# Kernel tuning notes

Measured on AMD Instinct MI355X. Metric: run time of the kernel, lower is better.

Reference implementation:

```python
import jax, jax.numpy as jnp
import numpy as np
import math

B = 64; H = 768; MAXL = 256; QL = 16  # query_lengths+1
LA = MAXL + QL  # 272 token-axis padded length for branch a
NC = 3


def _sa(x, qkv_w, qkv_b, scale):
    # x: [B, L, D]; qkv_w: [3, D, D] (query, key, value); returns [B, L, D]
    q = x @ qkv_w[0] + qkv_b[0]
    k = x @ qkv_w[1] + qkv_b[1]
    v = x @ qkv_w[2] + qkv_b[2]
    attn = jax.nn.softmax(jnp.einsum('bld,bmd->blm', q, k) * scale, axis=-1)
    return jnp.einsum('blm,bmd->bld', attn, v)


def setup_inputs() -> dict:
    key = jax.random.key(0)
    ks = jax.random.split(key, 16)
    rn = lambda k, s: jax.random.normal(k, s, jnp.float32) * 0.02
    return {
        'tokens': jax.random.normal(ks[0], (B, LA + 1, H), jnp.float32),
        'cls_tokens': jax.random.normal(ks[1], (B, MAXL + 1, H), jnp.float32),
        'a_qkv_w': rn(ks[2], (3, H, H)), 'a_qkv_b': jnp.zeros((3, H), jnp.float32),
        'af_qkv_w': rn(ks[3], (3, LA, LA)), 'af_qkv_b': jnp.zeros((3, LA), jnp.float32),
        'b_qkv_w': rn(ks[4], (3, H, H)), 'b_qkv_b': jnp.zeros((3, H), jnp.float32),
        'bf_qkv_w': rn(ks[5], (3, MAXL, MAXL)), 'bf_qkv_b': jnp.zeros((3, MAXL), jnp.float32),
        'atW_w': rn(ks[6], (H, 100)), 'atW_b': jnp.zeros((100,), jnp.float32),
        'afW_w': rn(ks[7], (H, 100)), 'afW_b': jnp.zeros((100,), jnp.float32),
        'btW_w': rn(ks[8], (H, 100)), 'btW_b': jnp.zeros((100,), jnp.float32),
        'bfW_w': rn(ks[9], (H, 100)), 'bfW_b': jnp.zeros((100,), jnp.float32),
        'aft_w': rn(ks[10], (10000, 1000)), 'aft_b': jnp.zeros((1000,), jnp.float32),
        'bft_w': rn(ks[11], (10000, 1000)), 'bft_b': jnp.zeros((1000,), jnp.float32),
        'fnn1_w': rn(ks[12], (2 * H, H)), 'fnn1_b': jnp.zeros((H,), jnp.float32),
        'fnn2_w': rn(ks[13], (H, NC)), 'fnn2_b': jnp.zeros((NC,), jnp.float32),
    }


def _forward(tokens, cls_tokens, a_qkv_w, a_qkv_b, af_qkv_w, af_qkv_b,
             b_qkv_w, b_qkv_b, bf_qkv_w, bf_qkv_b,
             atW_w, atW_b, afW_w, afW_b, btW_w, btW_b, bfW_w, bfW_b,
             aft_w, aft_b, bft_w, bft_b, fnn1_w, fnn1_b, fnn2_w, fnn2_b):
    CLS = tokens[:, 0, :]
    cls_CLS = cls_tokens[:, 0, :]
    xa = tokens[:, 1:, :]
    xa = jnp.pad(xa, ((0, 0), (0, LA - xa.shape[1]), (0, 0)))  # [B, LA, H]
    xb = cls_tokens[:, 1:, :]
    xb = jnp.pad(xb, ((0, 0), (0, MAXL - xb.shape[1]), (0, 0)))  # [B, MAXL, H]

    # branch a: token-axis self-attention (TSA) + feature-axis (FSA)
    aTSA = _sa(xa, a_qkv_w, a_qkv_b, 1.0 / math.sqrt(H))                        # [B, LA, H]
    aFSA = _sa(jnp.swapaxes(xa, 1, 2), af_qkv_w, af_qkv_b, 1.0 / math.sqrt(LA))  # [B, H, LA]
    aFSA = jnp.swapaxes(aFSA, 1, 2)                                              # [B, LA, H]
    aT = aTSA @ atW_w + atW_b   # [B, LA, 100]
    aF = aFSA @ afW_w + afW_b   # [B, LA, 100]
    a_TFSA = jnp.einsum('blm,bln->bmn', aT, aF).reshape(tokens.shape[0], 10000) @ aft_w + aft_b

    # branch b
    bTSA = _sa(xb, b_qkv_w, b_qkv_b, 1.0 / math.sqrt(H))
    bFSA = _sa(jnp.swapaxes(xb, 1, 2), bf_qkv_w, bf_qkv_b, 1.0 / math.sqrt(MAXL))
    bFSA = jnp.swapaxes(bFSA, 1, 2)
    bT = bTSA @ btW_w + btW_b
    bF = bFSA @ bfW_w + bfW_b
    b_TFSA = jnp.einsum('blm,bln->bmn', bT, bF).reshape(tokens.shape[0], 10000) @ bft_w + bft_b

    # classifier head (dropout is identity in eval mode)
    h = jnp.concatenate([CLS, cls_CLS], axis=1)
    predicts = (h @ fnn1_w + fnn1_b) @ fnn2_w + fnn2_b
    # concatenate the TFSA branches so the attention math stays live (original
    # computes them but returns only predicts; see notes)
    return jnp.concatenate([predicts, a_TFSA, b_TFSA], axis=1)


def reference(tokens, cls_tokens, a_qkv_w, a_qkv_b, af_qkv_w, af_qkv_b,
              b_qkv_w, b_qkv_b, bf_qkv_w, bf_qkv_b,
              atW_w, atW_b, afW_w, afW_b, btW_w, btW_b, bfW_w, bfW_b,
              aft_w, aft_b, bft_w, bft_b, fnn1_w, fnn1_b, fnn2_w, fnn2_b):
    return _forward(tokens, cls_tokens, a_qkv_w, a_qkv_b, af_qkv_w, af_qkv_b,
                    b_qkv_w, b_qkv_b, bf_qkv_w, bf_qkv_b,
                    atW_w, atW_b, afW_w, afW_b, btW_w, btW_b, bfW_w, bfW_b,
                    aft_w, aft_b, bft_w, bft_b, fnn1_w, fnn1_b, fnn2_w, fnn2_b)
```

## Files before the change

### kernel.cpp

```cpp
#include <hip/hip_runtime.h>
#include <hip/hip_bf16.h>
#include <math.h>

typedef __hip_bfloat16 bf16;
typedef __attribute__((ext_vector_type(8))) short bf16x8;
typedef __attribute__((ext_vector_type(4))) float f32x4;

typedef const void __attribute__((address_space(1)))* gptr_t;
typedef void __attribute__((address_space(3)))* lptr_t;

static __device__ __forceinline__ void gload16(const void* g, void* l) {
    __builtin_amdgcn_global_load_lds((gptr_t)g, (lptr_t)l, 16, 0, 0);
}

static __device__ __forceinline__ float tofl(float x) { return x; }
static __device__ __forceinline__ float tofl(bf16 x) { return __bfloat162float(x); }
static __device__ __forceinline__ float bfbits(unsigned short u) {
    return __uint_as_float(((unsigned)u) << 16);
}

template<int BN>
__global__ __launch_bounds__(256)
void gemm_mfma2(const bf16* __restrict__ A, const bf16* __restrict__ B,
                const float* __restrict__ bias, void* __restrict__ C, int c_mode,
                int M, int N, int K,
                long a_batch, long lda, int a_mod,
                long b_batch, long ldb, int b_div,
                long bias_stride, long c_batch, long c_row,
                float scale, int k_chunk,
                bf16* __restrict__ Ct, long t_zbatch, long t_batch, long t_ld,
                int t_colbase, int t_rowdiv)
{
    constexpr int BM = 128;
    constexpr int WN = BN / 2;
    constexpr int FM = 4, FN = WN / 16;
    constexpr int CP = BN + 4;
    constexpr int BUFS = (BM + BN) * 32;
    constexpr int NBUF = 3;
    constexpr int P = 2 + BN / 64;
    constexpr int ABSZ = NBUF * BUFS * 2;
    constexpr int CSZ  = BM * CP * 2;
    constexpr int SMSZ = (CSZ > ABSZ) ? CSZ : ABSZ;
    __shared__ __align__(16) char smem[SMSZ];
    short* SA = (short*)smem;

    const int gx = gridDim.x, gy = gridDim.y;
    const int nwg = gx * gy * (int)gridDim.z;
    const int orig = blockIdx.x + gx * (blockIdx.y + gy * blockIdx.z);
    const int qv = nwg >> 3, rv = nwg & 7;
    const int xcd = orig & 7, pos = orig >> 3;
    const int wg = (xcd < rv ? xcd * (qv + 1) : rv * (qv + 1) + (xcd - rv) * qv) + pos;
    const int bx = wg % gx, by = (wg / gx) % gy, bz = wg / (gx * gy);

    const int tid = threadIdx.x, w = tid >> 6, lane = tid & 63;
    const int wr = w >> 1, wc = w & 1, lrow = lane & 15, lch = lane >> 4;
    const bf16* Ab = A + (long)(bz % a_mod) * a_batch;
    const bf16* Bb = B + (long)(bz / b_div) * b_batch;
    const int i0 = by * BM, j0 = bx * BN;

    int kstart = 0, kend = K;
    if (k_chunk > 0) {
        kstart = bz * k_chunk;
        kend = kstart + k_chunk; if (kend > K) kend = K;
    }

    f32x4 acc[FM][FN];
#pragma unroll
    for (int m = 0; m < FM; ++m)
#pragma unroll
        for (int n = 0; n < FN; ++n) acc[m][n] = (f32x4){0.f, 0.f, 0.f, 0.f};

    const int srow = lane >> 2;
    const int schunk = ((lane & 3) ^ (srow & 3)) * 8;
    const int nt = (kend - kstart + 31) >> 5;
    const bf16x8 zero8 = {0, 0, 0, 0, 0, 0, 0, 0};

    auto stage = [&](int buf, int k0) {
        short* Asb = SA + buf * BUFS;
        short* Bsb = Asb + BM * 32;
#pragma unroll
        for (int u = 0; u < 2; ++u) {
            int row = w * 32 + u * 16 + srow;
            long gr = i0 + row; if (gr > M - 1) gr = M - 1;
            gload16(Ab + gr * lda + k0 + schunk, &Asb[(w * 32 + u * 16) * 32]);
        }
#pragma unroll
        for (int u = 0; u < BN / 64; ++u) {
            int row = w * (BN / 4) + u * 16 + srow;
            long gr = j0 + row; if (gr > N - 1) gr = N - 1;
            gload16(Bb + gr * ldb + k0 + schunk, &Bsb[(w * (BN / 4) + u * 16) * 32]);
        }
    };

    stage(0, kstart);
    if (nt > 1) stage(1, kstart + 32);

    for (int t = 0; t < nt; ++t) {
        if (t + 1 < nt)
            asm volatile("s_waitcnt vmcnt(%0)" :: "i"(P) : "memory");
        else
            asm volatile("s_waitcnt vmcnt(0)" ::: "memory");
        __builtin_amdgcn_s_barrier();
        __builtin_amdgcn_sched_barrier(0);

        if (t + 2 < nt) stage((t + 2) % NBUF, kstart + (t + 2) * 32);

        const int k0 = kstart + t * 32;
        short* Asb = SA + (t % NBUF) * BUFS;
        short* Bsb = Asb + BM * 32;
        bf16x8 af[FM], bfv[FN];
        const bool kok = (k0 + lch * 8) < kend;
#pragma unroll
        for (int m = 0; m < FM; ++m) {
            int row = wr * 64 + m * 16 + lrow;
            af[m] = *(const bf16x8*)&Asb[row * 32 + (lch ^ (row & 3)) * 8];
            if (!kok) af[m] = zero8;
        }
#pragma unroll
        for (int n = 0; n < FN; ++n) {
            int row = wc * WN + n * 16 + lrow;
            bfv[n] = *(const bf16x8*)&Bsb[row * 32 + (lch ^ (row & 3)) * 8];
            if (!kok) bfv[n] = zero8;
        }
#pragma unroll
        for (int m = 0; m < FM; ++m)
#pragma unroll
            for (int n = 0; n < FN; ++n)
                acc[m][n] = __builtin_amdgcn_mfma_f32_16x16x32_bf16(af[m], bfv[n], acc[m][n], 0, 0, 0);
    }

    const float* bp = bias ? (bias + (long)(bz / b_div) * bias_stride) : nullptr;

    if (c_mode == 1) {
#pragma unroll
        for (int n = 0; n < FN; ++n) {
            int cc = j0 + wc * WN + n * 16 + lrow;
            if (cc >= N) continue;
            float bv = bp ? bp[cc] : 0.f;
#pragma unroll
            for (int m = 0; m < FM; ++m) {
                int rbase = i0 + wr * 64 + m * 16 + lch * 4;
#pragma unroll
                for (int j = 0; j < 4; ++j) {
                    int r = rbase + j;
                    if (r >= M) continue;
                    ((float*)C)[(long)bz * c_batch + (long)r * c_row + cc] = acc[m][n][j] * scale + bv;
                }
            }
        }
        return;
    }

    __builtin_amdgcn_s_barrier();
    short* Cs = (short*)smem;
#pragma unroll
    for (int n = 0; n < FN; ++n) {
        int col = wc * WN + n * 16 + lrow;
        float bv = bp ? bp[(j0 + col < N) ? (j0 + col) : (N - 1)] : 0.f;
#pragma unroll
        for (int m = 0; m < FM; ++m) {
            int rb = wr * 64 + m * 16 + lch * 4;
#pragma unroll
            for (int j = 0; j < 4; ++j) {
                bf16 hv = __float2bfloat16(acc[m][n][j] * scale + bv);
                Cs[(rb + j) * CP + col] = *(short*)&hv;
            }
        }
    }
    __syncthreads();

    if (c_mode != 3) {
        constexpr int CHR = BN / 8;
        constexpr int CH = (BM * BN) / (256 * 8);
#pragma unroll
        for (int u = 0; u < CH; ++u) {
            int e = tid + u * 256;
            int row = e / CHR, c8 = (e % CHR) * 8;
            int r = i0 + row, cc = j0 + c8;
            if (r >= M) continue;
            if (c_mode == 2 && cc >= t_colbase) continue;
            bf16* dst = (bf16*)C + (long)bz * c_batch + (long)r * c_row + cc;
            if (cc + 8 <= N) {
                *(uint4*)dst = *(uint4*)&Cs[row * CP + c8];
            } else {
                for (int t2 = 0; t2 < 8; ++t2)
                    if (cc + t2 < N) dst[t2] = *(bf16*)&Cs[row * CP + c8 + t2];
            }
        }
    }

    if (c_mode >= 2) {
        constexpr int CHT = (BN * (BM / 8)) / 256;
#pragma unroll
        for (int u = 0; u < CHT; ++u) {
            int e = tid + u * 256;
            int col = e >> 4, r8 = e & 15;
            int j = j0 + col;
            int rb = i0 + r8 * 8;
            if (j < t_colbase || j >= N || rb >= M) continue;
            int b2 = rb / t_rowdiv;
            int rr = rb - b2 * t_rowdiv;
            long idx = (long)bz * t_zbatch + (long)b2 * t_batch + (long)(j - t_colbase) * t_ld + rr;
            uint4 val;
            unsigned short* vs = (unsigned short*)&val;
#pragma unroll
            for (int tt = 0; tt < 8; ++tt) vs[tt] = (unsigned short)Cs[(r8 * 8 + tt) * CP + col];
            *(uint4*)&Ct[idx] = val;
        }
    }
}

template<typename ST>
__global__ __launch_bounds__(256)
void transpose_to_bf16(const ST* __restrict__ src, bf16* __restrict__ dst,
                       int R, int C, long s_ld, long s_batch, long d_ld, long d_batch)
{
    __shared__ float t[32][33];
    const int z = blockIdx.z;
    const int tx = threadIdx.x & 31, ty = threadIdx.x >> 5;
    const int r0 = blockIdx.y << 5, c0 = blockIdx.x << 5;
    const ST* sb = src + (long)z * s_batch;
#pragma unroll
    for (int i = 0; i < 4; ++i) {
        int r = r0 + ty + i * 8, c = c0 + tx;
        if (r < R && c < C) t[ty + i * 8][tx] = tofl(sb[(long)r * s_ld + c]);
    }
    __syncthreads();
    bf16* db = dst + (long)z * d_batch;
#pragma unroll
    for (int i = 0; i < 4; ++i) {
        int dr = c0 + ty + i * 8, dc = r0 + tx;
        if (dr < C && dc < R) db[(long)dr * d_ld + dc] = __float2bfloat16(t[tx][ty + i * 8]);
    }
}

__global__ __launch_bounds__(256)
void convert_x(const float* __restrict__ src, bf16* __restrict__ dst, int L, int tokRows)
{
    long e = ((long)blockIdx.x * 256 + threadIdx.x) * 4;
    long per = (long)L * 768;
    long b = e / per, rem = e - b * per;
    const float4 v = *(const float4*)(src + b * (long)tokRows * 768 + 768 + rem);
    dst[e + 0] = __float2bfloat16(v.x);
    dst[e + 1] = __float2bfloat16(v.y);
    dst[e + 2] = __float2bfloat16(v.z);
    dst[e + 3] = __float2bfloat16(v.w);
}

__global__ __launch_bounds__(256)
void build_h(const float* __restrict__ tokens, const float* __restrict__ cls,
             bf16* __restrict__ hT, int tokRows, int clsRows)
{
    int idx = blockIdx.x * 256 + threadIdx.x;
    if (idx >= 64 * 1536) return;
    int b = idx / 1536, c = idx % 1536;
    float v = (c < 768) ? tokens[(long)b * tokRows * 768 + c]
                        : cls[(long)b * clsRows * 768 + (c - 768)];
    hT[idx] = __float2bfloat16(v);
}

__global__ __launch_bounds__(256)
void softmax_rows_bf16(bf16* __restrict__ S, long nrows, int rowlen)
{
    long row = (long)blockIdx.x * 4 + (threadIdx.x >> 6);
    if (row >= nrows) return;
    int lane = threadIdx.x & 63;
    uint4* p = (uint4*)(S + row * (long)rowlen);
    const int nch = rowlen >> 3;
    float v[2][8];
    float m = -3.4e38f;
#pragma unroll
    for (int i = 0; i < 2; ++i) {
        int c = lane + i * 64;
        if (c < nch) {
            uint4 raw = p[c];
            unsigned short* u = (unsigned short*)&raw;
#pragma unroll
            for (int j = 0; j < 8; ++j) { v[i][j] = bfbits(u[j]); m = fmaxf(m, v[i][j]); }
        }
    }
#pragma unroll
    for (int off = 32; off > 0; off >>= 1) m = fmaxf(m, __shfl_xor(m, off, 64));
    float s = 0.f;
#pragma unroll
    for (int i = 0; i < 2; ++i) {
        int c = lane + i * 64;
        if (c < nch) {
#pragma unroll
            for (int j = 0; j < 8; ++j) { v[i][j] = __expf(v[i][j] - m); s += v[i][j]; }
        }
    }
#pragma unroll
    for (int off = 32; off > 0; off >>= 1) s += __shfl_xor(s, off, 64);
    float inv = 1.f / s;
#pragma unroll
    for (int i = 0; i < 2; ++i) {
        int c = lane + i * 64;
        if (c < nch) {
            uint4 outv;
            unsigned short* u = (unsigned short*)&outv;
#pragma unroll
            for (int j = 0; j < 8; ++j) {
                bf16 hv = __float2bfloat16(v[i][j] * inv);
                u[j] = *(unsigned short*)&hv;
            }
            p[c] = outv;
        }
    }
}

__global__ __launch_bounds__(256)
void reduce_partials(const float* __restrict__ partial, const float* __restrict__ bias,
                     float* __restrict__ dst, int nz, int rows, int cols,
                     long dst_row_stride, long dst_col_off)
{
    int idx = blockIdx.x * 256 + threadIdx.x;
    if (idx >= rows * cols) return;
    int i = idx / cols, j = idx % cols;
    float s = bias ? bias[j] : 0.f;
    long rc = (long)rows * cols;
    for (int z = 0; z < nz; ++z) s += partial[(long)z * rc + idx];
    dst[(long)i * dst_row_stride + dst_col_off + j] = s;
}

__global__ __launch_bounds__(256)
void predicts_kernel(const float* __restrict__ h1, const float* __restrict__ w2,
                     const float* __restrict__ b2, float* __restrict__ out)
{
    int idx = threadIdx.x;
    if (idx >= 64 * 3) return;
    int b = idx / 3, c = idx % 3;
    float s = b2[c];
    const float* hr = h1 + (long)b * 768;
    for (int k = 0; k < 768; ++k) s = fmaf(hr[k], w2[k * 3 + c], s);
    out[(long)b * 2003 + c] = s;
}

static inline void mfma_launch(hipStream_t s, int bn,
    const bf16* A, const bf16* B, const float* bias, void* C, int c_mode,
    int M, int N, int K,
    long a_batch, long lda, int a_mod,
    long b_batch, long ldb, int b_div,
    long bias_stride, long c_batch, long c_row, float scale, int nz, int k_chunk = 0,
    bf16* Ct = nullptr, long t_zbatch = 0, long t_batch = 0, long t_ld = 0,
    int t_colbase = 0, int t_rowdiv = 8)
{
    if (bn == 128) {
        dim3 g((N + 127) / 128, (M + 127) / 128, nz);
        gemm_mfma2<128><<<g, dim3(256), 0, s>>>(A, B, bias, C, c_mode, M, N, K,
            a_batch, lda, a_mod, b_batch, ldb, b_div, bias_stride, c_batch, c_row, scale, k_chunk,
            Ct, t_zbatch, t_batch, t_ld, t_colbase, t_rowdiv);
    } else {
        dim3 g((N + 63) / 64, (M + 127) / 128, nz);
        gemm_mfma2<64><<<g, dim3(256), 0, s>>>(A, B, bias, C, c_mode, M, N, K,
            a_batch, lda, a_mod, b_batch, ldb, b_div, bias_stride, c_batch, c_row, scale, k_chunk,
            Ct, t_zbatch, t_batch, t_ld, t_colbase, t_rowdiv);
    }
}

extern "C" void kernel_launch(void* const* d_in, const int* in_sizes, int n_in,
                              void* d_out, int out_size, void* d_ws, size_t ws_size,
                              hipStream_t stream) {
    if (n_in < 26) return;
    const float* tokens     = (const float*)d_in[0];
    const float* cls_tokens = (const float*)d_in[1];
    const float* a_qkv_w  = (const float*)d_in[2];
    const float* a_qkv_b  = (const float*)d_in[3];
    const float* af_qkv_w = (const float*)d_in[4];
    const float* af_qkv_b = (const float*)d_in[5];
    const float* b_qkv_w  = (const float*)d_in[6];
    const float* b_qkv_b  = (const float*)d_in[7];
    const float* bf_qkv_w = (const float*)d_in[8];
    const float* bf_qkv_b = (const float*)d_in[9];
    const float* atW_w = (const float*)d_in[10];
    const float* atW_b = (const float*)d_in[11];
    const float* afW_w = (const float*)d_in[12];
    const float* afW_b = (const float*)d_in[13];
    const float* btW_w = (const float*)d_in[14];
    const float* btW_b = (const float*)d_in[15];
    const float* bfW_w = (const float*)d_in[16];
    const float* bfW_b = (const float*)d_in[17];
    const float* aft_w = (const float*)d_in[18];
    const float* aft_b = (const float*)d_in[19];
    const float* bft_w = (const float*)d_in[20];
    const float* bft_b = (const float*)d_in[21];
    const float* fnn1_w = (const float*)d_in[22];
    const float* fnn1_b = (const float*)d_in[23];
    const float* fnn2_w = (const float*)d_in[24];
    const float* fnn2_b = (const float*)d_in[25];
    float* outp = (float*)d_out;
    char* base = (char*)d_ws;

    const size_t OFF_QKV = 0;
    const size_t OFF_X   = 80216128;
    const size_t OFF_XT  = 106954880;
    const size_t OFF_O   = 133693632;
    const size_t OFF_SP  = 160432384;
    const size_t OFF_AT  = 179306816;
    const size_t OFF_AF  = 182788480;
    const size_t OFF_M   = 186270144;
    const size_t OFF_W   = 187550208;

    auto B16 = [&](size_t off) { return (bf16*)(base + off); };
    auto F32 = [&](size_t off) { return (float*)(base + off); };

    bf16* WqT  = B16(OFF_W);
    bf16* WfT  = (bf16*)(base + OFF_W + 3538944);
    bf16* atWt = (bf16*)(base + OFF_W + 3982848);
    bf16* afWt = (bf16*)(base + OFF_W + 4136448);

    auto phase = [&](int L, const float* tok, int tokRows,
                     const float* qkvW, const float* qkvB,
                     const float* fqkvW, const float* fqkvB,
                     const float* tWw, const float* tWb,
                     const float* fWw, const float* fWb,
                     const float* ftw, const float* ftb, long colOff)
    {
        const long LH = (long)L * 768;
        const long LL = (long)L * L;
        const int  L3 = 3 * L;
        bf16* qkv = B16(OFF_QKV);
        bf16* q = qkv, *k = qkv + 768;
        bf16* qf = qkv, *kf = qkv + L;
        bf16* xbf = B16(OFF_X);
        bf16* O   = B16(OFF_X);
        bf16* vfT = B16(OFF_X);
        bf16* xbT = B16(OFF_XT);
        bf16* Vt  = B16(OFF_O);
        bf16* OfT = B16(OFF_O);
        bf16* SP  = B16(OFF_SP);
        bf16* aTt = B16(OFF_AT);
        bf16* aFt = B16(OFF_AF);
        bf16* Mbf = B16(OFF_M);
        bf16* ftwT  = B16(OFF_QKV);
        float* PART = F32(OFF_QKV + 20000064);
        const int Lg = (L + 31) / 32;
        const float rsH = 1.0f / sqrtf(768.0f);
        const float rsL = 1.0f / sqrtf((float)L);

        convert_x<<<dim3((unsigned)(64L * L * 768 / 1024)), 256, 0, stream>>>(tok, xbf, L, tokRows);
        transpose_to_bf16<bf16><<<dim3(24, Lg, 64), 256, 0, stream>>>(xbf, xbT, L, 768, 768, LH, L, LH);
        transpose_to_bf16<float><<<dim3(24, 24, 3), 256, 0, stream>>>(qkvW, WqT, 768, 768, 768, 589824, 768, 589824);
        transpose_to_bf16<float><<<dim3(Lg, Lg, 3), 256, 0, stream>>>(fqkvW, WfT, L, L, L, LL, L, LL);
        transpose_to_bf16<float><<<dim3(4, 24, 1), 256, 0, stream>>>(tWw, atWt, 768, 100, 100, 0, 768, 0);
        transpose_to_bf16<float><<<dim3(4, 24, 1), 256, 0, stream>>>(fWw, afWt, 768, 100, 100, 0, 768, 0);

        mfma_launch(stream, 128, xbf, WqT, qkvB, qkv, 2, 64 * L, 2304, 768,
                    0, 768, 1, 0, 768, 1, 0, 0, 2304, 1.0f, 1, 0,
                    Vt, 0, LH, L, 1536, L);
        mfma_launch(stream, 128, q, k, nullptr, SP, 0, L, L, 768,
                    (long)L * 2304, 2304, 64, (long)L * 2304, 2304, 1, 0, LL, L, rsH, 64);
        softmax_rows_bf16<<<dim3((unsigned)((64L * L + 3) / 4)), 256, 0, stream>>>(SP, 64L * L, L);
        mfma_launch(stream, 128, SP, Vt, nullptr, O, 0, L, 768, L,
                    LL, L, 64, LH, L, 1, 0, LH, 768, 1.0f, 64);
        mfma_launch(stream, 64, O, atWt, tWb, nullptr, 3, 64 * L, 100, 768,
                    0, 768, 1, 0, 768, 1, 0, 0, 100, 1.0f, 1, 0,
                    aTt, 0, (long)100 * L, L, 0, L);

        mfma_launch(stream, 128, xbT, WfT, fqkvB, qkv, 2, 64 * 768, L3, L,
                    0, L, 1, 0, L, 1, 0, 0, L3, 1.0f, 1, 0,
                    vfT, 0, LH, 768, 2 * L, 768);
        for (int c = 0; c < 4; ++c) {
            long coA = (long)c * 16 * 768 * L3;
            long coV = (long)c * 16 * LH;
            mfma_launch(stream, 128, qf + coA, kf + coA, nullptr, SP, 0, 768, 768, L,
                        768L * L3, L3, 16, 768L * L3, L3, 1, 0, 589824, 768, rsL, 16);
            softmax_rows_bf16<<<dim3(16 * 768 / 4), 256, 0, stream>>>(SP, 16L * 768, 768);
            mfma_launch(stream, 128, SP, vfT + coV, nullptr, nullptr, 3, 768, L, 768,
                        589824, 768, 16, LH, 768, 1, 0, 0, 0, 1.0f, 16, 0,
                        OfT + coV, LH, 0, 768, 0, 768);
        }
        mfma_launch(stream, 64, OfT, afWt, fWb, nullptr, 3, 64 * L, 100, 768,
                    0, 768, 1, 0, 768, 1, 0, 0, 100, 1.0f, 1, 0,
                    aFt, 0, (long)100 * L, L, 0, L);

        mfma_launch(stream, 128, aTt, aFt, nullptr, Mbf, 0, 100, 100, L,
                    (long)100 * L, L, 64, (long)100 * L, L, 1, 0, 10000, 100, 1.0f, 64);
        transpose_to_bf16<float><<<dim3(32, 313, 1), 256, 0, stream>>>(ftw, ftwT, 10000, 1000, 1000, 0, 10000, 0);
        mfma_launch(stream, 128, Mbf, ftwT, nullptr, PART, 1, 64, 1000, 10000,
                    0, 10000, 1, 0, 10000, 1, 0, 64000, 1000, 1.0f, 32, 320);
        reduce_partials<<<dim3((64 * 1000 + 255) / 256), 256, 0, stream>>>(
            PART, ftb, outp, 32, 64, 1000, 2003, colOff);
    };

    phase(272, tokens,     273, a_qkv_w, a_qkv_b, af_qkv_w, af_qkv_b,
          atW_w, atW_b, afW_w, afW_b, aft_w, aft_b, 3);
    phase(256, cls_tokens, 257, b_qkv_w, b_qkv_b, bf_qkv_w, bf_qkv_b,
          btW_w, btW_b, bfW_w, bfW_b, bft_w, bft_b, 1003);

    bf16* hT     = B16(OFF_QKV);
    bf16* fnn1T  = (bf16*)(base + OFF_QKV + 262144);
    float* PARTF = F32(OFF_QKV + 2621504);
    float* h1    = F32(OFF_QKV + 3801216);
    build_h<<<dim3((64 * 1536 + 255) / 256), 256, 0, stream>>>(tokens, cls_tokens, hT, 273, 257);
    transpose_to_bf16<float><<<dim3(24, 48, 1), 256, 0, stream>>>(fnn1_w, fnn1T, 1536, 768, 768, 0, 1536, 0);
    mfma_launch(stream, 128, hT, fnn1T, nullptr, PARTF, 1, 64, 768, 1536,
                0, 1536, 1, 0, 1536, 1, 0, 49152, 768, 1.0f, 6, 256);
    reduce_partials<<<dim3((64 * 768 + 255) / 256), 256, 0, stream>>>(
        PARTF, fnn1_b, h1, 6, 64, 768, 768, 0);
    predicts_kernel<<<dim3(1), 256, 0, stream>>>(h1, fnn2_w, fnn2_b, outp);
}
```

Measured before the change: 1.107 ms.

## Split fused QKV GEMM and stage transposed epilogue in column-major LDS

Removes the mixed mode-2 epilogue that wrote Q/K row-major and V transposed in one GEMM. The projection now runs as two launches: a row-major Q|K GEMM and a separate V GEMM that writes only the transposed output. The transposed epilogue stores results into LDS column-major with packed 8-byte writes, so each output chunk is read back with one 16-byte LDS load instead of eight scalar gathers. The cost is an extra launch and re-reading the activations, and the narrower Q|K buffer changes the downstream leading dimensions.

```diff
diff --git a/kernel.cpp b/kernel.cpp
--- a/kernel.cpp
+++ b/kernel.cpp
@@ -29,18 +29,21 @@
                 long bias_stride, long c_batch, long c_row,
                 float scale, int k_chunk,
                 bf16* __restrict__ Ct, long t_zbatch, long t_batch, long t_ld,
-                int t_colbase, int t_rowdiv)
+                int t_rowdiv)
 {
     constexpr int BM = 128;
     constexpr int WN = BN / 2;
     constexpr int FM = 4, FN = WN / 16;
-    constexpr int CP = BN + 4;
+    constexpr int CP  = BN + 4;
+    constexpr int CPT = BM + 8;
     constexpr int BUFS = (BM + BN) * 32;
     constexpr int NBUF = 3;
     constexpr int P = 2 + BN / 64;
     constexpr int ABSZ = NBUF * BUFS * 2;
     constexpr int CSZ  = BM * CP * 2;
-    constexpr int SMSZ = (CSZ > ABSZ) ? CSZ : ABSZ;
+    constexpr int CTSZ = BN * CPT * 2;
+    constexpr int CMAX = (CSZ > CTSZ) ? CSZ : CTSZ;
+    constexpr int SMSZ = (CMAX > ABSZ) ? CMAX : ABSZ;
     __shared__ __align__(16) char smem[SMSZ];
     short* SA = (short*)smem;
 
@@ -153,23 +156,23 @@
 
     __builtin_amdgcn_s_barrier();
     short* Cs = (short*)smem;
-#pragma unroll
-    for (int n = 0; n < FN; ++n) {
-        int col = wc * WN + n * 16 + lrow;
-        float bv = bp ? bp[(j0 + col < N) ? (j0 + col) : (N - 1)] : 0.f;
-#pragma unroll
-        for (int m = 0; m < FM; ++m) {
-            int rb = wr * 64 + m * 16 + lch * 4;
-#pragma unroll
-            for (int j = 0; j < 4; ++j) {
-                bf16 hv = __float2bfloat16(acc[m][n][j] * scale + bv);
-                Cs[(rb + j) * CP + col] = *(short*)&hv;
+
+    if (c_mode == 0) {
+#pragma unroll
+        for (int n = 0; n < FN; ++n) {
+            int col = wc * WN + n * 16 + lrow;
+            float bv = bp ? bp[(j0 + col < N) ? (j0 + col) : (N - 1)] : 0.f;
+#pragma unroll
+            for (int m = 0; m < FM; ++m) {
+                int rb = wr * 64 + m * 16 + lch * 4;
+#pragma unroll
+                for (int j = 0; j < 4; ++j) {
+                    bf16 hv = __float2bfloat16(acc[m][n][j] * scale + bv);
+                    Cs[(rb + j) * CP + col] = *(short*)&hv;
+                }
             }
         }
-    }
-    __syncthreads();
-
-    if (c_mode != 3) {
+        __syncthreads();
         constexpr int CHR = BN / 8;
         constexpr int CH = (BM * BN) / (256 * 8);
 #pragma unroll
@@ -178,7 +181,6 @@
             int row = e / CHR, c8 = (e % CHR) * 8;
             int r = i0 + row, cc = j0 + c8;
             if (r >= M) continue;
-            if (c_mode == 2 && cc >= t_colbase) continue;
             bf16* dst = (bf16*)C + (long)bz * c_batch + (long)r * c_row + cc;
             if (cc + 8 <= N) {
                 *(uint4*)dst = *(uint4*)&Cs[row * CP + c8];
@@ -187,9 +189,25 @@
                     if (cc + t2 < N) dst[t2] = *(bf16*)&Cs[row * CP + c8 + t2];
             }
         }
-    }
-
-    if (c_mode >= 2) {
+    } else {
+#pragma unroll
+        for (int n = 0; n < FN; ++n) {
+            int col = wc * WN + n * 16 + lrow;
+            float bv = bp ? bp[(j0 + col < N) ? (j0 + col) : (N - 1)] : 0.f;
+#pragma unroll
+            for (int m = 0; m < FM; ++m) {
+                int rb = wr * 64 + m * 16 + lch * 4;
+                uint2 pk;
+                unsigned short* ps = (unsigned short*)&pk;
+#pragma unroll
+                for (int j = 0; j < 4; ++j) {
+                    bf16 hv = __float2bfloat16(acc[m][n][j] * scale + bv);
+                    ps[j] = *(unsigned short*)&hv;
+                }
+                *(uint2*)&Cs[col * CPT + rb] = pk;
+            }
+        }
+        __syncthreads();
         constexpr int CHT = (BN * (BM / 8)) / 256;
 #pragma unroll
         for (int u = 0; u < CHT; ++u) {
@@ -197,15 +215,11 @@
             int col = e >> 4, r8 = e & 15;
             int j = j0 + col;
             int rb = i0 + r8 * 8;
-            if (j < t_colbase || j >= N || rb >= M) continue;
+            if (j >= N || rb >= M) continue;
             int b2 = rb / t_rowdiv;
             int rr = rb - b2 * t_rowdiv;
-            long idx = (long)bz * t_zbatch + (long)b2 * t_batch + (long)(j - t_colbase) * t_ld + rr;
-            uint4 val;
-            unsigned short* vs = (unsigned short*)&val;
-#pragma unroll
-            for (int tt = 0; tt < 8; ++tt) vs[tt] = (unsigned short)Cs[(r8 * 8 + tt) * CP + col];
-            *(uint4*)&Ct[idx] = val;
+            long idx = (long)bz * t_zbatch + (long)b2 * t_batch + (long)j * t_ld + rr;
+            *(uint4*)&Ct[idx] = *(uint4*)&Cs[col * CPT + r8 * 8];
         }
     }
 }
@@ -343,18 +357,18 @@
     long b_batch, long ldb, int b_div,
     long bias_stride, long c_batch, long c_row, float scale, int nz, int k_chunk = 0,
     bf16* Ct = nullptr, long t_zbatch = 0, long t_batch = 0, long t_ld = 0,
-    int t_colbase = 0, int t_rowdiv = 8)
+    int t_rowdiv = 8)
 {
     if (bn == 128) {
         dim3 g((N + 127) / 128, (M + 127) / 128, nz);
         gemm_mfma2<128><<<g, dim3(256), 0, s>>>(A, B, bias, C, c_mode, M, N, K,
             a_batch, lda, a_mod, b_batch, ldb, b_div, bias_stride, c_batch, c_row, scale, k_chunk,
-            Ct, t_zbatch, t_batch, t_ld, t_colbase, t_rowdiv);
+            Ct, t_zbatch, t_batch, t_ld, t_rowdiv);
     } else {
         dim3 g((N + 63) / 64, (M + 127) / 128, nz);
         gemm_mfma2<64><<<g, dim3(256), 0, s>>>(A, B, bias, C, c_mode, M, N, K,
             a_batch, lda, a_mod, b_batch, ldb, b_div, bias_stride, c_batch, c_row, scale, k_chunk,
-            Ct, t_zbatch, t_batch, t_ld, t_colbase, t_rowdiv);
+            Ct, t_zbatch, t_batch, t_ld, t_rowdiv);
     }
 }
 
@@ -418,7 +432,7 @@
     {
         const long LH = (long)L * 768;
         const long LL = (long)L * L;
-        const int  L3 = 3 * L;
+        const int  L2 = 2 * L;
         bf16* qkv = B16(OFF_QKV);
         bf16* q = qkv, *k = qkv + 768;
         bf16* qf = qkv, *kf = qkv + L;
@@ -445,34 +459,38 @@
         transpose_to_bf16<float><<<dim3(4, 24, 1), 256, 0, stream>>>(tWw, atWt, 768, 100, 100, 0, 768, 0);
         transpose_to_bf16<float><<<dim3(4, 24, 1), 256, 0, stream>>>(fWw, afWt, 768, 100, 100, 0, 768, 0);
 
-        mfma_launch(stream, 128, xbf, WqT, qkvB, qkv, 2, 64 * L, 2304, 768,
-                    0, 768, 1, 0, 768, 1, 0, 0, 2304, 1.0f, 1, 0,
-                    Vt, 0, LH, L, 1536, L);
+        mfma_launch(stream, 128, xbf, WqT, qkvB, qkv, 0, 64 * L, 1536, 768,
+                    0, 768, 1, 0, 768, 1, 0, 0, 1536, 1.0f, 1);
+        mfma_launch(stream, 128, xbf, WqT + 1536L * 768, qkvB + 1536, nullptr, 3, 64 * L, 768, 768,
+                    0, 768, 1, 0, 768, 1, 0, 0, 0, 1.0f, 1, 0,
+                    Vt, 0, LH, L, L);
         mfma_launch(stream, 128, q, k, nullptr, SP, 0, L, L, 768,
-                    (long)L * 2304, 2304, 64, (long)L * 2304, 2304, 1, 0, LL, L, rsH, 64);
+                    (long)L * 1536, 1536, 64, (long)L * 1536, 1536, 1, 0, LL, L, rsH, 64);
         softmax_rows_bf16<<<dim3((unsigned)((64L * L + 3) / 4)), 256, 0, stream>>>(SP, 64L * L, L);
         mfma_launch(stream, 128, SP, Vt, nullptr, O, 0, L, 768, L,
                     LL, L, 64, LH, L, 1, 0, LH, 768, 1.0f, 64);
         mfma_launch(stream, 64, O, atWt, tWb, nullptr, 3, 64 * L, 100, 768,
                     0, 768, 1, 0, 768, 1, 0, 0, 100, 1.0f, 1, 0,
-                    aTt, 0, (long)100 * L, L, 0, L);
-
-        mfma_launch(stream, 128, xbT, WfT, fqkvB, qkv, 2, 64 * 768, L3, L,
-                    0, L, 1, 0, L, 1, 0, 0, L3, 1.0f, 1, 0,
-                    vfT, 0, LH, 768, 2 * L, 768);
+                    aTt, 0, (long)100 * L, L, L);
+
+        mfma_launch(stream, 128, xbT, WfT, fqkvB, qkv, 0, 64 * 768, L2, L,
+                    0, L, 1, 0, L, 1, 0, 0, L2, 1.0f, 1);
+        mfma_launch(stream, 128, xbT, WfT + (long)L2 * L, fqkvB + L2, nullptr, 3, 64 * 768, L, L,
+                    0, L, 1, 0, L, 1, 0, 0, 0, 1.0f, 1, 0,
+                    vfT, 0, LH, 768, 768);
         for (int c = 0; c < 4; ++c) {
-            long coA = (long)c * 16 * 768 * L3;
+            long coA = (long)c * 16 * 768 * L2;
             long coV = (long)c * 16 * LH;
             mfma_launch(stream, 128, qf + coA, kf + coA, nullptr, SP, 0, 768, 768, L,
-                        768L * L3, L3, 16, 768L * L3, L3, 1, 0, 589824, 768, rsL, 16);
+                        768L * L2, L2, 16, 768L * L2, L2, 1, 0, 589824, 768, rsL, 16);
             softmax_rows_bf16<<<dim3(16 * 768 / 4), 256, 0, stream>>>(SP, 16L * 768, 768);
             mfma_launch(stream, 128, SP, vfT + coV, nullptr, nullptr, 3, 768, L, 768,
                         589824, 768, 16, LH, 768, 1, 0, 0, 0, 1.0f, 16, 0,
-                        OfT + coV, LH, 0, 768, 0, 768);
+                        OfT + coV, LH, 0, 768, 768);
         }
         mfma_launch(stream, 64, OfT, afWt, fWb, nullptr, 3, 64 * L, 100, 768,
                     0, 768, 1, 0, 768, 1, 0, 0, 100, 1.0f, 1, 0,
-                    aFt, 0, (long)100 * L, L, 0, L);
+                    aFt, 0, (long)100 * L, L, L);
 
         mfma_launch(stream, 128, aTt, aFt, nullptr, Mbf, 0, 100, 100, L,
                     (long)100 * L, L, 64, (long)100 * L, L, 1, 0, 10000, 100, 1.0f, 64);
```

Result: no change. 1.118 ms (+0.9%).
